# Optimization experiments

Hardware: AMD Instinct MI355X
Metric: run time of the kernel (lower is better)

The kernel has to match this reference:

```python
import jax, jax.numpy as jnp
import numpy as np

G = 8          # grid_size
N = G * G      # 64 nodes
DEG = 17       # neighbors per node for 8x8 sudoku (2x4 boxes)
STEPS = 32
H = 96         # hidden_dim
E = 16         # embed_size
B = 16         # batch


def sudoku_edges():
    # row (7) + col (7) + 2x4 box (7) neighbors, set-union -> 17 per node
    idx = np.arange(N).reshape(G, G)
    nb = []
    for j in range(N):
        r, c = j // G, j % G
        br, bc = (r // 2) * 2, (c // 4) * 4
        s = set(idx[r, :].tolist()) | set(idx[:, c].tolist()) | set(idx[br:br + 2, bc:bc + 4].flatten().tolist())
        s.discard(j)
        nb.append(sorted(s))
    return np.asarray(nb, dtype=np.int32)  # [64, 17]


def setup_inputs() -> dict:
    key = jax.random.key(0)
    ks = jax.random.split(key, 16)
    sc = 0.05
    inp = {
        "x": jax.random.randint(ks[0], (B, G, G), 0, G + 1),            # given digits, 0 = blank
        "target": jax.random.randint(ks[1], (B, G, G), 0, G) + 1,       # solutions in 1..8
        "edges": jnp.asarray(sudoku_edges()),                            # [64, 17] int32
        "digit_emb": jax.random.normal(ks[2], (G + 1, E), jnp.float32) * sc,
        "row_emb": jax.random.normal(ks[3], (G, E), jnp.float32) * sc,
        "col_emb": jax.random.normal(ks[4], (G, E), jnp.float32) * sc,
        "in0_W": jax.random.normal(ks[5], (3 * E, H), jnp.float32) * sc,
        "in0_b": jnp.zeros((H,), jnp.float32),
        "in_Ws": jax.random.normal(ks[6], (3, H, H), jnp.float32) * sc,
        "in_bs": jnp.zeros((3, H), jnp.float32),
        "msg0_W": jax.random.normal(ks[7], (2 * H, H), jnp.float32) * sc,
        "msg0_b": jnp.zeros((H,), jnp.float32),
        "msg_Ws": jax.random.normal(ks[8], (3, H, H), jnp.float32) * sc,
        "msg_bs": jnp.zeros((3, H), jnp.float32),
        "W_ih": jax.random.normal(ks[9], (2 * H, 4 * H), jnp.float32) * sc,
        "W_hh": jax.random.normal(ks[10], (H, 4 * H), jnp.float32) * sc,
        "b_ih": jnp.zeros((4 * H,), jnp.float32),
        "b_hh": jnp.zeros((4 * H,), jnp.float32),
        "pred_W": jax.random.normal(ks[11], (H, G), jnp.float32) * sc,
        "pred_b": jnp.zeros((G,), jnp.float32),
    }
    return inp


def _mlp(z, W0, b0, Ws, bs):
    # Linear -> ReLU -> Linear -> ReLU -> Linear -> ReLU -> Linear (def_MLP)
    z = jax.nn.relu(z @ W0 + b0)
    z = jax.nn.relu(z @ Ws[0] + bs[0])
    z = jax.nn.relu(z @ Ws[1] + bs[1])
    return z @ Ws[2] + bs[2]


def reference(x, target, edges, digit_emb, row_emb, col_emb,
              in0_W, in0_b, in_Ws, in_bs,
              msg0_W, msg0_b, msg_Ws, msg_bs,
              W_ih, W_hh, b_ih, b_hh, pred_W, pred_b):
    bsz = x.shape[0]
    xf = x.reshape(bsz, N)
    tgt = target.reshape(bsz, N) - 1                      # labels 0..7

    de = digit_emb[xf]                                    # [B,64,E]
    re = row_emb[jnp.repeat(jnp.arange(G), G)]            # [64,E]
    ce = col_emb[jnp.tile(jnp.arange(G), G)]              # [64,E]
    feat = jnp.concatenate([de,
                            jnp.broadcast_to(re[None], (bsz, N, E)),
                            jnp.broadcast_to(ce[None], (bsz, N, E))], axis=-1)
    xin = _mlp(feat, in0_W, in0_b, in_Ws, in_bs)          # [B,64,H]

    h0 = jnp.zeros((bsz, N, H), jnp.float32)
    s0 = jnp.zeros((bsz * N, H), jnp.float32)

    def step(carry, _):
        h, s, loss = carry
        # gather-by-edge message passing
        h_edges = h[:, edges]                                             # [B,64,17,H]
        h_self = jnp.broadcast_to(h[:, :, None, :], (bsz, N, DEG, H))
        msg = _mlp(jnp.concatenate([h_edges, h_self], -1),
                   msg0_W, msg0_b, msg_Ws, msg_bs).sum(axis=2)            # [B,64,H]
        # LSTMCell update
        lstm_in = jnp.concatenate([msg, xin], -1).reshape(bsz * N, 2 * H)
        gates = lstm_in @ W_ih + b_ih + h.reshape(bsz * N, H) @ W_hh + b_hh
        i, f, g, o = jnp.split(gates, 4, axis=-1)
        s2 = jax.nn.sigmoid(f) * s + jax.nn.sigmoid(i) * jnp.tanh(g)
        h2 = (jax.nn.sigmoid(o) * jnp.tanh(s2)).reshape(bsz, N, H)
        # per-step prediction / loss / accuracy
        logp = jax.nn.log_softmax(h2 @ pred_W + pred_b, axis=-1)          # [B,64,8]
        pred = jnp.argmax(logp, axis=-1)
        acc = jnp.mean(jnp.all(pred == tgt, axis=1).astype(jnp.float32))
        loss_n = -jnp.sum(jnp.take_along_axis(logp, tgt[..., None], -1)) / (bsz * N)
        return (h2, s2, loss + loss_n), acc

    (h, s, loss), accs = jax.lax.scan(step, (h0, s0, jnp.float32(0.0)), None, length=STEPS)
    loss = loss / STEPS
    final_pred = jnp.argmax(h @ pred_W + pred_b, axis=-1)                 # [B,64]
    return loss, accs, final_pred
```

## Files before the change

### kernel.cpp

```cpp
#include <hip/hip_runtime.h>

#define DEG 17
#define NSTEPS 32
#define HD 96

#define WS_U0     0
#define WS_BAR    196608
#define WS_U1     196864
#define WS_XIN    393472
#define WS_GX     491776
#define WS_LOSSP  884992
#define WS_CNTP   901376

#define W1L    0
#define W2L    9216
#define MSGB   18432
#define M0B    18720
#define PRW    18816
#define MSGH4  19584
#define GATES4 20352
#define H2T4   21888
#define SLC4   22272
#define GX4    22656
#define LGT    24192
#define NBRI   24224
#define BARC   24304
#define VBASE  24320
#define VSTR   7888
#define VZ1    0
#define VZ2    3840
#define VS3T   7680
#define SMTOT  (VBASE + 2*VSTR)

__global__ void init_kernel(
    const int* __restrict__ x,
    const float* __restrict__ digit_emb,
    const float* __restrict__ row_emb,
    const float* __restrict__ col_emb,
    const float* __restrict__ in0_W,
    const float* __restrict__ in0_b,
    const float* __restrict__ in_Ws,
    const float* __restrict__ in_bs,
    const float* __restrict__ msg0_b,
    float* __restrict__ xin,
    float* __restrict__ u0)
{
  const int node = blockIdx.x;
  const int j = threadIdx.x;
  const int n = node & 63;
  const int r = n >> 3, c = n & 7;
  __shared__ float feat[48];
  __shared__ float za[HD];
  __shared__ float zb[HD];
  if (j < 16)      feat[j] = digit_emb[x[node]*16 + j];
  else if (j < 32) feat[j] = row_emb[r*16 + (j-16)];
  else if (j < 48) feat[j] = col_emb[c*16 + (j-32)];
  u0[node*192 + 96 + j] = msg0_b[j];
  __syncthreads();
  float a = in0_b[j];
  for (int k = 0; k < 48; ++k) a = fmaf(feat[k], in0_W[k*HD + j], a);
  za[j] = fmaxf(a, 0.f);
  __syncthreads();
  a = in_bs[j];
  for (int k = 0; k < HD; ++k) a = fmaf(za[k], in_Ws[k*HD + j], a);
  zb[j] = fmaxf(a, 0.f);
  __syncthreads();
  a = in_bs[HD + j];
  for (int k = 0; k < HD; ++k) a = fmaf(zb[k], in_Ws[9216 + k*HD + j], a);
  za[j] = fmaxf(a, 0.f);
  __syncthreads();
  a = in_bs[2*HD + j];
  for (int k = 0; k < HD; ++k) a = fmaf(za[k], in_Ws[2*9216 + k*HD + j], a);
  xin[node*HD + j] = a;
}

__global__ __launch_bounds__(384) void gx_kernel(
    const float* __restrict__ xin, const float* __restrict__ W_ih,
    const float* __restrict__ b_ih, const float* __restrict__ b_hh,
    float* __restrict__ gx)
{
  __shared__ float xs[4*HD];
  const int tid = threadIdx.x;
  const int base = blockIdx.x * 4;
  {
    const int m = tid / HD, k = tid - m*HD;
    xs[m*HD + k] = xin[(base+m)*HD + k];
  }
  __syncthreads();
  const int j = tid;
  float a0 = b_ih[j] + b_hh[j], a1 = a0, a2 = a0, a3 = a0;
  for (int k = 0; k < HD; ++k) {
    const float w = W_ih[(96+k)*384 + j];
    a0 = fmaf(xs[k], w, a0);
    a1 = fmaf(xs[HD+k], w, a1);
    a2 = fmaf(xs[2*HD+k], w, a2);
    a3 = fmaf(xs[3*HD+k], w, a3);
  }
  gx[(base+0)*384 + j] = a0;
  gx[(base+1)*384 + j] = a1;
  gx[(base+2)*384 + j] = a2;
  gx[(base+3)*384 + j] = a3;
}

__device__ __forceinline__ void vbar(int* c, int want) {
  if ((threadIdx.x & 63) == 0)
    __hip_atomic_fetch_add(c, 1, __ATOMIC_RELEASE, __HIP_MEMORY_SCOPE_WORKGROUP);
  while (__hip_atomic_load(c, __ATOMIC_ACQUIRE, __HIP_MEMORY_SCOPE_WORKGROUP) < want)
    __builtin_amdgcn_s_sleep(1);
}

__global__ __launch_bounds__(512, 1) void solve_kernel(
    const int* __restrict__ edges,
    const float* __restrict__ msg0_W, const float* __restrict__ msg0_b,
    const float* __restrict__ msg_Ws, const float* __restrict__ msg_bs,
    const float* __restrict__ W_ih, const float* __restrict__ W_hh,
    const float* __restrict__ pred_W, const float* __restrict__ pred_b,
    const int* __restrict__ target,
    const float* __restrict__ gx,
    float* __restrict__ u0, float* __restrict__ u1,
    int* bar,
    float* __restrict__ lossP, int* __restrict__ cntP,
    float* __restrict__ final_pred_out)
{
  __shared__ float sm[SMTOT];

  const int tid = threadIdx.x;
  const int vb  = tid >> 8;
  const int vt  = tid & 255;
  const int blk = blockIdx.x;
  const int bb  = blk & 15;
  const int grp = blk >> 4;
  const int base = bb*64 + grp*4;

  float* const vs = sm + VBASE + vb*VSTR;
  int* const nbrs = (int*)(sm + NBRI);
  int* const vbc = (int*)(sm + BARC) + vb;

  for (int i = tid*4; i < 9216; i += 2048) {
    *(float4*)&sm[W1L + i] = *(const float4*)&msg_Ws[i];
    *(float4*)&sm[W2L + i] = *(const float4*)&msg_Ws[9216 + i];
  }
  if (tid < 288) sm[MSGB + tid] = msg_bs[tid];
  if (tid < 96)  sm[M0B + tid]  = msg0_b[tid];
  if (tid < 2)   ((int*)(sm + BARC))[tid] = 0;
  for (int i = tid; i < 768; i += 512) sm[PRW + i] = pred_W[i];
  #pragma unroll
  for (int t = 0; t < 3; ++t) {
    const int idx = t*512 + tid;
    sm[GX4 + idx] = gx[base*384 + idx];
  }
  if (tid < 384) {
    sm[SLC4 + tid] = 0.f;
    sm[MSGH4 + 384 + tid] = 0.f;
  }
  if (tid < 80) {
    const int m = tid / 20, r = tid % 20;
    nbrs[tid] = (r < DEG) ? (bb*64 + edges[(grp*4 + m)*DEG + r])*192 : -1;
  }
  __syncthreads();

  const float* uP = u0;
  float*       uN = u1;
  int vph = 0;

  for (int st = 0; st < NSTEPS; ++st) {
    if (vt < 240) {
      const int row = vt % 40;
      const int kh  = vt / 40;
      const int m = row / 20;
      const int k0 = kh * 16;
      const int nb = nbrs[vb*40 + row];
      if (nb >= 0) {
        const float* ue = uP + nb + k0;
        const float* us = uP + (base + vb*2 + m)*192 + 96 + k0;
        #pragma unroll
        for (int t = 0; t < 4; ++t) {
          const float4 a = *(const float4*)(ue + 4*t);
          const float4 b = *(const float4*)(us + 4*t);
          vs[VZ1 + (k0+4*t+0)*40 + row] = fmaxf(a.x + b.x, 0.f);
          vs[VZ1 + (k0+4*t+1)*40 + row] = fmaxf(a.y + b.y, 0.f);
          vs[VZ1 + (k0+4*t+2)*40 + row] = fmaxf(a.z + b.z, 0.f);
          vs[VZ1 + (k0+4*t+3)*40 + row] = fmaxf(a.w + b.w, 0.f);
        }
      } else {
        #pragma unroll
        for (int t = 0; t < 16; ++t) vs[VZ1 + (k0+t)*40 + row] = 0.f;
      }
    } else {
      const int i = vt - 240;
      #pragma unroll
      for (int t = 0; t < 12; ++t) vs[VS3T + i*12 + t] = 0.f;
    }
    vph += 4; vbar(vbc, vph);

    if (vt < 240) {
      const int jg = vt % 24, dg = vt / 24;
      const int j4 = jg*4, d4 = dg*4;
      float acc[4][4] = {{0.f}};
      #pragma unroll 4
      for (int k = 0; k < 96; ++k) {
        const float4 z = *(const float4*)&vs[VZ1 + k*40 + d4];
        const float4 w = *(const float4*)&sm[W1L + k*96 + j4];
        const float ze[4] = {z.x, z.y, z.z, z.w};
        const float we[4] = {w.x, w.y, w.z, w.w};
        #pragma unroll
        for (int dd = 0; dd < 4; ++dd)
          #pragma unroll
          for (int jj = 0; jj < 4; ++jj)
            acc[dd][jj] = fmaf(ze[dd], we[jj], acc[dd][jj]);
      }
      #pragma unroll
      for (int jj = 0; jj < 4; ++jj) {
        const float b1 = sm[MSGB + j4 + jj];
        float4 q;
        q.x = fmaxf(acc[0][jj] + b1, 0.f);
        q.y = fmaxf(acc[1][jj] + b1, 0.f);
        q.z = fmaxf(acc[2][jj] + b1, 0.f);
        q.w = fmaxf(acc[3][jj] + b1, 0.f);
        *(float4*)&vs[VZ2 + (j4+jj)*40 + d4] = q;
      }
    }
    vph += 4; vbar(vbc, vph);

    if (vt < 240) {
      const int jg = vt % 24, dg = vt / 24;
      const int j4 = jg*4, d4 = dg*4;
      float acc[4][4] = {{0.f}};
      #pragma unroll 4
      for (int k = 0; k < 96; ++k) {
        const float4 z = *(const float4*)&vs[VZ2 + k*40 + d4];
        const float4 w = *(const float4*)&sm[W2L + k*96 + j4];
        const float ze[4] = {z.x, z.y, z.z, z.w};
        const float we[4] = {w.x, w.y, w.z, w.w};
        #pragma unroll
        for (int dd = 0; dd < 4; ++dd)
          #pragma unroll
          for (int jj = 0; jj < 4; ++jj)
            acc[dd][jj] = fmaf(ze[dd], we[jj], acc[dd][jj]);
      }
      const int nd = d4 / 20;
      const int r0 = d4 - nd*20;
      #pragma unroll
      for (int jj = 0; jj < 4; ++jj) {
        const float b2 = sm[MSGB + 96 + j4 + jj];
        float p = 0.f;
        #pragma unroll
        for (int dd = 0; dd < 4; ++dd)
          if (r0 + dd < DEG) p += fmaxf(acc[dd][jj] + b2, 0.f);
        atomicAdd(&vs[VS3T + (j4+jj)*2 + nd], p);
      }
    }
    vph += 4; vbar(vbc, vph);

    if (vt < 192) {
      const int jg = vt % 24, kq = vt / 24;
      const int j4 = jg*4, k0 = kq*12;
      const float* W3 = msg_Ws + 2*9216;
      float acc[2][4] = {{0.f}};
      #pragma unroll
      for (int kk = 0; kk < 12; ++kk) {
        const int k = k0 + kk;
        const float2 sv = *(const float2*)&vs[VS3T + k*2];
        const float4 wv = *(const float4*)&W3[k*96 + j4];
        const float se[2] = {sv.x, sv.y};
        const float we[4] = {wv.x, wv.y, wv.z, wv.w};
        #pragma unroll
        for (int m = 0; m < 2; ++m)
          #pragma unroll
          for (int jj = 0; jj < 4; ++jj)
            acc[m][jj] = fmaf(se[m], we[jj], acc[m][jj]);
      }
      #pragma unroll
      for (int m = 0; m < 2; ++m) {
        float4 q = {acc[m][0], acc[m][1], acc[m][2], acc[m][3]};
        *(float4*)&vs[VZ1 + (kq*2 + m)*96 + j4] = q;
      }
    }
    vph += 4; vbar(vbc, vph);
    if (vt < 192) {
      const int m = vt / 96, j = vt % 96;
      float v = 17.f * sm[MSGB + 192 + j];
      #pragma unroll
      for (int kq = 0; kq < 8; ++kq) v += vs[VZ1 + (kq*2 + m)*96 + j];
      sm[MSGH4 + j*4 + vb*2 + m] = v;
    }
    __syncthreads();

    {
      const int jg = vt & 31, kq = vt >> 5;
      const int j6 = vb*192 + jg*6;
      const int jl = jg*6;
      const int k0 = kq*24;
      const float* Wb = (kq < 4) ? (W_ih + (size_t)k0*384 + j6)
                                 : (W_hh + (size_t)(k0-96)*384 + j6);
      float acc[4][6] = {{0.f}};
      #pragma unroll 4
      for (int kk = 0; kk < 24; ++kk) {
        const float4 mv = *(const float4*)&sm[MSGH4 + (k0+kk)*4];
        const float* wp = Wb + (size_t)kk*384;
        const float2 wa = *(const float2*)wp;
        const float2 wb2 = *(const float2*)(wp + 2);
        const float2 wc = *(const float2*)(wp + 4);
        const float me[4] = {mv.x, mv.y, mv.z, mv.w};
        const float we[6] = {wa.x, wa.y, wb2.x, wb2.y, wc.x, wc.y};
        #pragma unroll
        for (int m = 0; m < 4; ++m)
          #pragma unroll
          for (int jj = 0; jj < 6; ++jj)
            acc[m][jj] = fmaf(me[m], we[jj], acc[m][jj]);
      }
      #pragma unroll
      for (int m = 0; m < 4; ++m) {
        float2 qa = {acc[m][0], acc[m][1]};
        float2 qb = {acc[m][2], acc[m][3]};
        float2 qc = {acc[m][4], acc[m][5]};
        *(float2*)&vs[VZ1 + (kq*4 + m)*192 + jl]     = qa;
        *(float2*)&vs[VZ1 + (kq*4 + m)*192 + jl + 2] = qb;
        *(float2*)&vs[VZ1 + (kq*4 + m)*192 + jl + 4] = qc;
      }
    }
    __syncthreads();
    {
      #pragma unroll
      for (int t = 0; t < 3; ++t) {
        const int idx = t*512 + tid;
        const int m = idx / 384, j = idx - m*384;
        const int vbh = (j >= 192) ? 1 : 0;
        const int jl = j - vbh*192;
        const float* pb = sm + VBASE + vbh*VSTR;
        float g = sm[GX4 + idx];
        #pragma unroll
        for (int kq = 0; kq < 8; ++kq) g += pb[VZ1 + (kq*4 + m)*192 + jl];
        sm[GATES4 + idx] = g;
      }
    }
    __syncthreads();

    if (tid < 384) {
      const int m = tid / 96, hj = tid - m*96;
      const float gi = sm[GATES4 + m*384 + hj];
      const float gf = sm[GATES4 + m*384 + 96 + hj];
      const float gg = sm[GATES4 + m*384 + 192 + hj];
      const float go = sm[GATES4 + m*384 + 288 + hj];
      const float sv = sm[SLC4 + tid];
      const float ig = 1.f/(1.f + expf(-gi));
      const float fg = 1.f/(1.f + expf(-gf));
      const float cg = tanhf(gg);
      const float og = 1.f/(1.f + expf(-go));
      const float s2 = fg*sv + ig*cg;
      const float h2 = og*tanhf(s2);
      sm[SLC4 + tid] = s2;
      sm[H2T4 + hj*4 + m] = h2;
      sm[MSGH4 + (96+hj)*4 + m] = h2;
    }
    __syncthreads();

    {
      const int jg = vt & 15, kq = vt >> 4;
      const int j6 = jg*6;
      const float* Wb = (vb == 0) ? (msg0_W + j6) : (msg0_W + 9216 + j6);
      const int k0 = kq*6;
      float acc[4][6] = {{0.f}};
      #pragma unroll
      for (int kk = 0; kk < 6; ++kk) {
        const int k = k0 + kk;
        const float4 hv = *(const float4*)&sm[H2T4 + k*4];
        const float* wp = Wb + k*96;
        const float2 wa = *(const float2*)wp;
        const float2 wb2 = *(const float2*)(wp + 2);
        const float2 wc = *(const float2*)(wp + 4);
        const float he[4] = {hv.x, hv.y, hv.z, hv.w};
        const float we[6] = {wa.x, wa.y, wb2.x, wb2.y, wc.x, wc.y};
        #pragma unroll
        for (int m = 0; m < 4; ++m)
          #pragma unroll
          for (int jj = 0; jj < 6; ++jj)
            acc[m][jj] = fmaf(he[m], we[jj], acc[m][jj]);
      }
      #pragma unroll
      for (int m = 0; m < 4; ++m) {
        float2 qa = {acc[m][0], acc[m][1]};
        float2 qb = {acc[m][2], acc[m][3]};
        float2 qc = {acc[m][4], acc[m][5]};
        *(float2*)&vs[VZ1 + (kq*4 + m)*96 + j6]     = qa;
        *(float2*)&vs[VZ1 + (kq*4 + m)*96 + j6 + 2] = qb;
        *(float2*)&vs[VZ1 + (kq*4 + m)*96 + j6 + 4] = qc;
      }
    }
    __syncthreads();
    if (tid < 384) {
      #pragma unroll
      for (int t = 0; t < 2; ++t) {
        const int idx = t*384 + tid;
        const int m = idx / 192, j = idx - m*192;
        const int vbh = (j >= 96) ? 1 : 0;
        const int jl = j - vbh*96;
        const float* pb = sm + VBASE + vbh*VSTR;
        float v = vbh ? sm[M0B + jl] : 0.f;
        #pragma unroll
        for (int kq = 0; kq < 16; ++kq) v += pb[VZ1 + (kq*4 + m)*96 + jl];
        uN[(base+m)*192 + j] = v;
      }
    } else {
      const int t2 = tid - 384;
      const int m = t2 >> 5, c = (t2 >> 2) & 7, kq2 = t2 & 3;
      float p = 0.f;
      #pragma unroll
      for (int kk = 0; kk < 24; ++kk) {
        const int k = kq2*24 + kk;
        p = fmaf(sm[H2T4 + k*4 + m], sm[PRW + k*8 + c], p);
      }
      p += __shfl_xor(p, 1);
      p += __shfl_xor(p, 2);
      if (kq2 == 0) sm[LGT + m*8 + c] = p + pred_b[c];
    }
    __syncthreads();

    if (tid < 4) {
      const int m = tid;
      const int node = base + m;
      float mx = sm[LGT + m*8];
      int pred = 0;
      #pragma unroll
      for (int c = 1; c < 8; ++c) {
        const float v = sm[LGT + m*8 + c];
        if (v > mx) { mx = v; pred = c; }
      }
      float sum = 0.f;
      #pragma unroll
      for (int c = 0; c < 8; ++c) sum += expf(sm[LGT + m*8 + c] - mx);
      const float lse = mx + logf(sum);
      const int tgt = target[node] - 1;
      sm[LGT + 16 + m] = lse - sm[LGT + m*8 + tgt];
      sm[LGT + 20 + m] = (pred == tgt) ? 1.f : 0.f;
      if (st == NSTEPS-1) final_pred_out[node] = (float)pred;
      if (m == 0) {
        lossP[st*256 + blk] = sm[LGT+16] + sm[LGT+17] + sm[LGT+18] + sm[LGT+19];
        cntP[st*256 + blk] = (int)(sm[LGT+20] + sm[LGT+21] + sm[LGT+22] + sm[LGT+23]);
      }
    }

    if (st < NSTEPS-1) {
      __syncthreads();
      if (tid == 0) {
        __hip_atomic_fetch_add(&bar[bb*16], 1, __ATOMIC_RELEASE, __HIP_MEMORY_SCOPE_AGENT);
        const int want = 16*(st+1);
        while (__hip_atomic_load(&bar[bb*16], __ATOMIC_RELAXED, __HIP_MEMORY_SCOPE_AGENT) < want)
          __builtin_amdgcn_s_sleep(2);
        __threadfence();
      }
      __syncthreads();
      const float* tp = uP; uP = uN; uN = (float*)tp;
    }
  }
}

__global__ void finalize_kernel(const float* __restrict__ lossP,
                                const int* __restrict__ cntP,
                                float* __restrict__ out)
{
  __shared__ float sl[32];
  const int tid = threadIdx.x;
  const int st = tid >> 3, q = tid & 7;
  float lsum = 0.f;
  for (int i = 0; i < 32; ++i) lsum += lossP[st*256 + q*32 + i];
  lsum += __shfl_xor(lsum, 1);
  lsum += __shfl_xor(lsum, 2);
  lsum += __shfl_xor(lsum, 4);
  if (q == 0) sl[st] = lsum;
  float okc = 0.f;
  #pragma unroll
  for (int t = 0; t < 2; ++t) {
    const int bbat = q + 8*t;
    int c = 0;
    for (int i = 0; i < 16; ++i) c += cntP[st*256 + i*16 + bbat];
    okc += (c == 64) ? 1.f : 0.f;
  }
  okc += __shfl_xor(okc, 1);
  okc += __shfl_xor(okc, 2);
  okc += __shfl_xor(okc, 4);
  if (q == 0) out[1 + st] = okc / 16.f;
  __syncthreads();
  if (tid == 0) {
    float tot = 0.f;
    for (int i = 0; i < 32; ++i) tot += sl[i];
    out[0] = tot / (1024.f * (float)NSTEPS);
  }
}

extern "C" void kernel_launch(void* const* d_in, const int* in_sizes, int n_in,
                              void* d_out, int out_size, void* d_ws, size_t ws_size,
                              hipStream_t stream) {
  const int*   x         = (const int*)  d_in[0];
  const int*   target    = (const int*)  d_in[1];
  const int*   edges     = (const int*)  d_in[2];
  const float* digit_emb = (const float*)d_in[3];
  const float* row_emb   = (const float*)d_in[4];
  const float* col_emb   = (const float*)d_in[5];
  const float* in0_W     = (const float*)d_in[6];
  const float* in0_b     = (const float*)d_in[7];
  const float* in_Ws     = (const float*)d_in[8];
  const float* in_bs     = (const float*)d_in[9];
  const float* msg0_W    = (const float*)d_in[10];
  const float* msg0_b    = (const float*)d_in[11];
  const float* msg_Ws    = (const float*)d_in[12];
  const float* msg_bs    = (const float*)d_in[13];
  const float* W_ih      = (const float*)d_in[14];
  const float* W_hh      = (const float*)d_in[15];
  const float* b_ih      = (const float*)d_in[16];
  const float* b_hh      = (const float*)d_in[17];
  const float* pred_W    = (const float*)d_in[18];
  const float* pred_b    = (const float*)d_in[19];

  float* ws    = (float*)d_ws;
  float* u0    = ws + WS_U0;
  int*   bar   = (int*)(ws + WS_BAR);
  float* u1    = ws + WS_U1;
  float* xin   = ws + WS_XIN;
  float* gxb   = ws + WS_GX;
  float* lossP = ws + WS_LOSSP;
  int*   cntP  = (int*)(ws + WS_CNTP);

  hipMemsetAsync(d_ws, 0, (size_t)(196608 + 256)*sizeof(float), stream);

  init_kernel<<<1024, HD, 0, stream>>>(x, digit_emb, row_emb, col_emb,
                                       in0_W, in0_b, in_Ws, in_bs,
                                       msg0_b, xin, u0);
  gx_kernel<<<256, 384, 0, stream>>>(xin, W_ih, b_ih, b_hh, gxb);

  float* outp = (float*)d_out;
  solve_kernel<<<256, 512, 0, stream>>>(
      edges, msg0_W, msg0_b, msg_Ws, msg_bs,
      W_ih, W_hh, pred_W, pred_b, target, gxb,
      u0, u1, bar, lossP, cntP, outp + 1 + NSTEPS);

  finalize_kernel<<<1, 256, 0, stream>>>(lossP, cntP, outp);
}
```

Before: 1.044 ms.

## Double solve_kernel block size to 1024 threads, halving per-thread work

The persistent solve kernel goes from 512 to 1024 threads per block, and every phase is re-partitioned so each thread does half the work. This covers the edge gather, the two message MLP layers, the edge-sum reduction, the gate matmuls and the msg0 projection. The edge-sum accumulator is split into two slots to reduce atomic contention, and scratch space grows to match. The goal is more latency hiding across the per-step chain of small matmuls, at the cost of smaller per-thread register tiles (less reuse), more barrier participants and heavier register pressure at 1024 threads.

```diff
diff --git a/kernel.cpp b/kernel.cpp
--- a/kernel.cpp
+++ b/kernel.cpp
@@ -26,7 +26,7 @@
 #define NBRI   24224
 #define BARC   24304
 #define VBASE  24320
-#define VSTR   7888
+#define VSTR   8080
 #define VZ1    0
 #define VZ2    3840
 #define VS3T   7680
@@ -109,7 +109,7 @@
     __builtin_amdgcn_s_sleep(1);
 }
 
-__global__ __launch_bounds__(512, 1) void solve_kernel(
+__global__ __launch_bounds__(1024) void solve_kernel(
     const int* __restrict__ edges,
     const float* __restrict__ msg0_W, const float* __restrict__ msg0_b,
     const float* __restrict__ msg_Ws, const float* __restrict__ msg_bs,
@@ -125,8 +125,8 @@
   __shared__ float sm[SMTOT];
 
   const int tid = threadIdx.x;
-  const int vb  = tid >> 8;
-  const int vt  = tid & 255;
+  const int vb  = tid >> 9;
+  const int vt  = tid & 511;
   const int blk = blockIdx.x;
   const int bb  = blk & 15;
   const int grp = blk >> 4;
@@ -136,18 +136,18 @@
   int* const nbrs = (int*)(sm + NBRI);
   int* const vbc = (int*)(sm + BARC) + vb;
 
-  for (int i = tid*4; i < 9216; i += 2048) {
+  for (int i = tid*4; i < 9216; i += 4096) {
     *(float4*)&sm[W1L + i] = *(const float4*)&msg_Ws[i];
     *(float4*)&sm[W2L + i] = *(const float4*)&msg_Ws[9216 + i];
   }
   if (tid < 288) sm[MSGB + tid] = msg_bs[tid];
   if (tid < 96)  sm[M0B + tid]  = msg0_b[tid];
   if (tid < 2)   ((int*)(sm + BARC))[tid] = 0;
-  for (int i = tid; i < 768; i += 512) sm[PRW + i] = pred_W[i];
+  if (tid < 768) sm[PRW + tid] = pred_W[tid];
   #pragma unroll
-  for (int t = 0; t < 3; ++t) {
-    const int idx = t*512 + tid;
-    sm[GX4 + idx] = gx[base*384 + idx];
+  for (int t = 0; t < 2; ++t) {
+    const int idx = t*1024 + tid;
+    if (idx < 1536) sm[GX4 + idx] = gx[base*384 + idx];
   }
   if (tid < 384) {
     sm[SLC4 + tid] = 0.f;
@@ -164,17 +164,17 @@
   int vph = 0;
 
   for (int st = 0; st < NSTEPS; ++st) {
-    if (vt < 240) {
+    if (vt < 480) {
       const int row = vt % 40;
-      const int kh  = vt / 40;
+      const int kc  = vt / 40;
       const int m = row / 20;
-      const int k0 = kh * 16;
+      const int k0 = kc * 8;
       const int nb = nbrs[vb*40 + row];
       if (nb >= 0) {
         const float* ue = uP + nb + k0;
         const float* us = uP + (base + vb*2 + m)*192 + 96 + k0;
         #pragma unroll
-        for (int t = 0; t < 4; ++t) {
+        for (int t = 0; t < 2; ++t) {
           const float4 a = *(const float4*)(ue + 4*t);
           const float4 b = *(const float4*)(us + 4*t);
           vs[VZ1 + (k0+4*t+0)*40 + row] = fmaxf(a.x + b.x, 0.f);
@@ -184,27 +184,27 @@
         }
       } else {
         #pragma unroll
-        for (int t = 0; t < 16; ++t) vs[VZ1 + (k0+t)*40 + row] = 0.f;
+        for (int t = 0; t < 8; ++t) vs[VZ1 + (k0+t)*40 + row] = 0.f;
       }
     } else {
-      const int i = vt - 240;
+      const int i = vt - 480;
       #pragma unroll
       for (int t = 0; t < 12; ++t) vs[VS3T + i*12 + t] = 0.f;
     }
-    vph += 4; vbar(vbc, vph);
-
-    if (vt < 240) {
+    vph += 8; vbar(vbc, vph);
+
+    if (vt < 480) {
       const int jg = vt % 24, dg = vt / 24;
-      const int j4 = jg*4, d4 = dg*4;
-      float acc[4][4] = {{0.f}};
+      const int j4 = jg*4, d2 = dg*2;
+      float acc[2][4] = {{0.f}};
       #pragma unroll 4
       for (int k = 0; k < 96; ++k) {
-        const float4 z = *(const float4*)&vs[VZ1 + k*40 + d4];
+        const float2 z = *(const float2*)&vs[VZ1 + k*40 + d2];
         const float4 w = *(const float4*)&sm[W1L + k*96 + j4];
-        const float ze[4] = {z.x, z.y, z.z, z.w};
+        const float ze[2] = {z.x, z.y};
         const float we[4] = {w.x, w.y, w.z, w.w};
         #pragma unroll
-        for (int dd = 0; dd < 4; ++dd)
+        for (int dd = 0; dd < 2; ++dd)
           #pragma unroll
           for (int jj = 0; jj < 4; ++jj)
             acc[dd][jj] = fmaf(ze[dd], we[jj], acc[dd][jj]);
@@ -212,57 +212,55 @@
       #pragma unroll
       for (int jj = 0; jj < 4; ++jj) {
         const float b1 = sm[MSGB + j4 + jj];
-        float4 q;
+        float2 q;
         q.x = fmaxf(acc[0][jj] + b1, 0.f);
         q.y = fmaxf(acc[1][jj] + b1, 0.f);
-        q.z = fmaxf(acc[2][jj] + b1, 0.f);
-        q.w = fmaxf(acc[3][jj] + b1, 0.f);
-        *(float4*)&vs[VZ2 + (j4+jj)*40 + d4] = q;
-      }
-    }
-    vph += 4; vbar(vbc, vph);
-
-    if (vt < 240) {
+        *(float2*)&vs[VZ2 + (j4+jj)*40 + d2] = q;
+      }
+    }
+    vph += 8; vbar(vbc, vph);
+
+    if (vt < 480) {
       const int jg = vt % 24, dg = vt / 24;
-      const int j4 = jg*4, d4 = dg*4;
-      float acc[4][4] = {{0.f}};
+      const int j4 = jg*4, d2 = dg*2;
+      float acc[2][4] = {{0.f}};
       #pragma unroll 4
       for (int k = 0; k < 96; ++k) {
-        const float4 z = *(const float4*)&vs[VZ2 + k*40 + d4];
+        const float2 z = *(const float2*)&vs[VZ2 + k*40 + d2];
         const float4 w = *(const float4*)&sm[W2L + k*96 + j4];
-        const float ze[4] = {z.x, z.y, z.z, z.w};
+        const float ze[2] = {z.x, z.y};
         const float we[4] = {w.x, w.y, w.z, w.w};
         #pragma unroll
-        for (int dd = 0; dd < 4; ++dd)
+        for (int dd = 0; dd < 2; ++dd)
           #pragma unroll
           for (int jj = 0; jj < 4; ++jj)
             acc[dd][jj] = fmaf(ze[dd], we[jj], acc[dd][jj]);
       }
-      const int nd = d4 / 20;
-      const int r0 = d4 - nd*20;
+      const int nd = dg / 10, slot = dg & 1;
+      const int r0 = d2 - nd*20;
       #pragma unroll
       for (int jj = 0; jj < 4; ++jj) {
         const float b2 = sm[MSGB + 96 + j4 + jj];
         float p = 0.f;
         #pragma unroll
-        for (int dd = 0; dd < 4; ++dd)
+        for (int dd = 0; dd < 2; ++dd)
           if (r0 + dd < DEG) p += fmaxf(acc[dd][jj] + b2, 0.f);
-        atomicAdd(&vs[VS3T + (j4+jj)*2 + nd], p);
-      }
-    }
-    vph += 4; vbar(vbc, vph);
-
-    if (vt < 192) {
+        atomicAdd(&vs[VS3T + (j4+jj)*4 + nd*2 + slot], p);
+      }
+    }
+    vph += 8; vbar(vbc, vph);
+
+    if (vt < 384) {
       const int jg = vt % 24, kq = vt / 24;
-      const int j4 = jg*4, k0 = kq*12;
+      const int j4 = jg*4, k0 = kq*6;
       const float* W3 = msg_Ws + 2*9216;
       float acc[2][4] = {{0.f}};
       #pragma unroll
-      for (int kk = 0; kk < 12; ++kk) {
+      for (int kk = 0; kk < 6; ++kk) {
         const int k = k0 + kk;
-        const float2 sv = *(const float2*)&vs[VS3T + k*2];
+        const float4 sv = *(const float4*)&vs[VS3T + k*4];
+        const float se[2] = {sv.x + sv.y, sv.z + sv.w};
         const float4 wv = *(const float4*)&W3[k*96 + j4];
-        const float se[2] = {sv.x, sv.y};
         const float we[4] = {wv.x, wv.y, wv.z, wv.w};
         #pragma unroll
         for (int m = 0; m < 2; ++m)
@@ -276,62 +274,58 @@
         *(float4*)&vs[VZ1 + (kq*2 + m)*96 + j4] = q;
       }
     }
-    vph += 4; vbar(vbc, vph);
+    vph += 8; vbar(vbc, vph);
     if (vt < 192) {
       const int m = vt / 96, j = vt % 96;
       float v = 17.f * sm[MSGB + 192 + j];
       #pragma unroll
-      for (int kq = 0; kq < 8; ++kq) v += vs[VZ1 + (kq*2 + m)*96 + j];
+      for (int kq = 0; kq < 16; ++kq) v += vs[VZ1 + (kq*2 + m)*96 + j];
       sm[MSGH4 + j*4 + vb*2 + m] = v;
     }
     __syncthreads();
 
     {
-      const int jg = vt & 31, kq = vt >> 5;
-      const int j6 = vb*192 + jg*6;
-      const int jl = jg*6;
+      const int jg = vt & 63, kq = vt >> 6;
+      const int j3 = jg*3;
       const int k0 = kq*24;
-      const float* Wb = (kq < 4) ? (W_ih + (size_t)k0*384 + j6)
-                                 : (W_hh + (size_t)(k0-96)*384 + j6);
-      float acc[4][6] = {{0.f}};
+      const float* Wb = (kq < 4) ? (W_ih + (size_t)k0*384 + vb*192 + j3)
+                                 : (W_hh + (size_t)(k0-96)*384 + vb*192 + j3);
+      float acc[4][3] = {{0.f}};
       #pragma unroll 4
       for (int kk = 0; kk < 24; ++kk) {
         const float4 mv = *(const float4*)&sm[MSGH4 + (k0+kk)*4];
         const float* wp = Wb + (size_t)kk*384;
-        const float2 wa = *(const float2*)wp;
-        const float2 wb2 = *(const float2*)(wp + 2);
-        const float2 wc = *(const float2*)(wp + 4);
+        const float w0 = wp[0], w1 = wp[1], w2 = wp[2];
         const float me[4] = {mv.x, mv.y, mv.z, mv.w};
-        const float we[6] = {wa.x, wa.y, wb2.x, wb2.y, wc.x, wc.y};
-        #pragma unroll
-        for (int m = 0; m < 4; ++m)
-          #pragma unroll
-          for (int jj = 0; jj < 6; ++jj)
-            acc[m][jj] = fmaf(me[m], we[jj], acc[m][jj]);
+        #pragma unroll
+        for (int m = 0; m < 4; ++m) {
+          acc[m][0] = fmaf(me[m], w0, acc[m][0]);
+          acc[m][1] = fmaf(me[m], w1, acc[m][1]);
+          acc[m][2] = fmaf(me[m], w2, acc[m][2]);
+        }
       }
       #pragma unroll
       for (int m = 0; m < 4; ++m) {
-        float2 qa = {acc[m][0], acc[m][1]};
-        float2 qb = {acc[m][2], acc[m][3]};
-        float2 qc = {acc[m][4], acc[m][5]};
-        *(float2*)&vs[VZ1 + (kq*4 + m)*192 + jl]     = qa;
-        *(float2*)&vs[VZ1 + (kq*4 + m)*192 + jl + 2] = qb;
-        *(float2*)&vs[VZ1 + (kq*4 + m)*192 + jl + 4] = qc;
+        vs[VZ1 + (kq*4 + m)*192 + j3]     = acc[m][0];
+        vs[VZ1 + (kq*4 + m)*192 + j3 + 1] = acc[m][1];
+        vs[VZ1 + (kq*4 + m)*192 + j3 + 2] = acc[m][2];
       }
     }
     __syncthreads();
     {
       #pragma unroll
-      for (int t = 0; t < 3; ++t) {
-        const int idx = t*512 + tid;
-        const int m = idx / 384, j = idx - m*384;
-        const int vbh = (j >= 192) ? 1 : 0;
-        const int jl = j - vbh*192;
-        const float* pb = sm + VBASE + vbh*VSTR;
-        float g = sm[GX4 + idx];
-        #pragma unroll
-        for (int kq = 0; kq < 8; ++kq) g += pb[VZ1 + (kq*4 + m)*192 + jl];
-        sm[GATES4 + idx] = g;
+      for (int t = 0; t < 2; ++t) {
+        const int idx = t*1024 + tid;
+        if (idx < 1536) {
+          const int m = idx / 384, j = idx - m*384;
+          const int vbh = (j >= 192) ? 1 : 0;
+          const int jl = j - vbh*192;
+          const float* pb = sm + VBASE + vbh*VSTR;
+          float g = sm[GX4 + idx];
+          #pragma unroll
+          for (int kq = 0; kq < 8; ++kq) g += pb[VZ1 + (kq*4 + m)*192 + jl];
+          sm[GATES4 + idx] = g;
+        }
       }
     }
     __syncthreads();
@@ -356,53 +350,44 @@
     __syncthreads();
 
     {
-      const int jg = vt & 15, kq = vt >> 4;
-      const int j6 = jg*6;
-      const float* Wb = (vb == 0) ? (msg0_W + j6) : (msg0_W + 9216 + j6);
+      const int jg = vt & 31, kq = vt >> 5;
+      const int j3 = jg*3;
+      const float* Wb = (vb == 0) ? (msg0_W + j3) : (msg0_W + 9216 + j3);
       const int k0 = kq*6;
-      float acc[4][6] = {{0.f}};
+      float acc[4][3] = {{0.f}};
       #pragma unroll
       for (int kk = 0; kk < 6; ++kk) {
         const int k = k0 + kk;
         const float4 hv = *(const float4*)&sm[H2T4 + k*4];
         const float* wp = Wb + k*96;
-        const float2 wa = *(const float2*)wp;
-        const float2 wb2 = *(const float2*)(wp + 2);
-        const float2 wc = *(const float2*)(wp + 4);
+        const float w0 = wp[0], w1 = wp[1], w2 = wp[2];
         const float he[4] = {hv.x, hv.y, hv.z, hv.w};
-        const float we[6] = {wa.x, wa.y, wb2.x, wb2.y, wc.x, wc.y};
-        #pragma unroll
-        for (int m = 0; m < 4; ++m)
-          #pragma unroll
-          for (int jj = 0; jj < 6; ++jj)
-            acc[m][jj] = fmaf(he[m], we[jj], acc[m][jj]);
+        #pragma unroll
+        for (int m = 0; m < 4; ++m) {
+          acc[m][0] = fmaf(he[m], w0, acc[m][0]);
+          acc[m][1] = fmaf(he[m], w1, acc[m][1]);
+          acc[m][2] = fmaf(he[m], w2, acc[m][2]);
+        }
       }
       #pragma unroll
       for (int m = 0; m < 4; ++m) {
-        float2 qa = {acc[m][0], acc[m][1]};
-        float2 qb = {acc[m][2], acc[m][3]};
-        float2 qc = {acc[m][4], acc[m][5]};
-        *(float2*)&vs[VZ1 + (kq*4 + m)*96 + j6]     = qa;
-        *(float2*)&vs[VZ1 + (kq*4 + m)*96 + j6 + 2] = qb;
-        *(float2*)&vs[VZ1 + (kq*4 + m)*96 + j6 + 4] = qc;
+        vs[VZ1 + (kq*4 + m)*96 + j3]     = acc[m][0];
+        vs[VZ1 + (kq*4 + m)*96 + j3 + 1] = acc[m][1];
+        vs[VZ1 + (kq*4 + m)*96 + j3 + 2] = acc[m][2];
       }
     }
     __syncthreads();
-    if (tid < 384) {
-      #pragma unroll
-      for (int t = 0; t < 2; ++t) {
-        const int idx = t*384 + tid;
-        const int m = idx / 192, j = idx - m*192;
-        const int vbh = (j >= 96) ? 1 : 0;
-        const int jl = j - vbh*96;
-        const float* pb = sm + VBASE + vbh*VSTR;
-        float v = vbh ? sm[M0B + jl] : 0.f;
-        #pragma unroll
-        for (int kq = 0; kq < 16; ++kq) v += pb[VZ1 + (kq*4 + m)*96 + jl];
-        uN[(base+m)*192 + j] = v;
-      }
-    } else {
-      const int t2 = tid - 384;
+    if (tid < 768) {
+      const int m = tid / 192, j = tid - m*192;
+      const int vbh = (j >= 96) ? 1 : 0;
+      const int jl = j - vbh*96;
+      const float* pb = sm + VBASE + vbh*VSTR;
+      float v = vbh ? sm[M0B + jl] : 0.f;
+      #pragma unroll
+      for (int kq = 0; kq < 16; ++kq) v += pb[VZ1 + (kq*4 + m)*96 + jl];
+      uN[(base+m)*192 + j] = v;
+    } else if (tid < 896) {
+      const int t2 = tid - 768;
       const int m = t2 >> 5, c = (t2 >> 2) & 7, kq2 = t2 & 3;
       float p = 0.f;
       #pragma unroll
@@ -529,7 +514,7 @@
   gx_kernel<<<256, 384, 0, stream>>>(xin, W_ih, b_ih, b_hh, gxb);
 
   float* outp = (float*)d_out;
-  solve_kernel<<<256, 512, 0, stream>>>(
+  solve_kernel<<<256, 1024, 0, stream>>>(
       edges, msg0_W, msg0_b, msg_Ws, msg_bs,
       W_ih, W_hh, pred_W, pred_b, target, gxb,
       u0, u1, bar, lossP, cntP, outp + 1 + NSTEPS);
```

Measured after the change: 1.498 ms. 1.43x slower.
